# Kernel tuning notes

Hardware: AMD Instinct MI355X
Metric: run time of the kernel (lower is better)

The kernel has to match this reference:

```python
import jax, jax.numpy as jnp
import numpy as np

N_NODES = 100_000
N_EDGES = 1_200_000


def _lap_weights(src, dst, attr, n):
    # PyG get_laplacian(sym) + ChebConv scaling with lambda_max=2.0:
    # L_hat = (2/lmax)(I - D^-1/2 A D^-1/2) - I = -D^-1/2 A D^-1/2 (zero diagonal)
    deg = jnp.zeros((n,), attr.dtype).at[src].add(attr)
    dis = jnp.where(deg > 0, jax.lax.rsqrt(jnp.maximum(deg, 1e-30)), 0.0)
    return -(dis[src] * attr * dis[dst])


def _prop(x, src, dst, lw, n):
    # y_i = sum_{(j->i)} lw_e * x_j   (gather -> scale -> scatter-add)
    return jnp.zeros((n, x.shape[1]), x.dtype).at[dst].add(lw[:, None] * x[src])


def _cheb(x, src, dst, lw, W, b):
    # W: [K, F_in, F_out]; Tx0 = x, Tx1 = L_hat x (K<=2 here)
    out = x @ W[0]
    if W.shape[0] > 1:
        tx1 = _prop(x, src, dst, lw, x.shape[0])
        out = out + tx1 @ W[1]
    return out + b


def setup_inputs() -> dict:
    key = jax.random.key(0)
    ks = jax.random.split(key, 11)
    x = jax.random.normal(ks[0], (N_NODES, 20), jnp.float32)
    edge_index = jax.random.randint(ks[1], (2, N_EDGES), 0, N_NODES, jnp.int32)
    attr = jax.random.uniform(ks[2], (N_EDGES,), jnp.float32)
    def glorot(k, shape):
        fan = shape[-2] + shape[-1]
        return jax.random.normal(k, shape, jnp.float32) * jnp.sqrt(2.0 / fan)
    return {
        "x": x, "edge_index": edge_index, "attr": attr,
        "w1": glorot(ks[3], (1, 20, 32)), "b1": jnp.zeros((32,), jnp.float32),
        "w2": glorot(ks[4], (2, 32, 64)), "b2": jnp.zeros((64,), jnp.float32),
        "w3": glorot(ks[5], (2, 64, 2)), "b3": jnp.zeros((2,), jnp.float32),
        "gate_w": glorot(ks[6], (2, 1)), "gate_b": jnp.zeros((1,), jnp.float32),
    }


def reference(x, edge_index, attr, w1, b1, w2, b2, w3, b3, gate_w, gate_b):
    n = x.shape[0]
    src, dst = edge_index[0], edge_index[1]
    lw = _lap_weights(src, dst, attr, n)
    h = jax.nn.leaky_relu(_cheb(x, src, dst, lw, w1, b1))   # [N, 32]
    h = jax.nn.leaky_relu(_cheb(h, src, dst, lw, w2, b2))   # [N, 64]
    h = _cheb(h, src, dst, lw, w3, b3)                       # [N, 2]
    # GlobalAttention with batch = zeros (single graph): softmax over nodes
    gate = jax.nn.softmax(h @ gate_w + gate_b, axis=0)       # [N, 1]
    pooled = jnp.sum(gate * h, axis=0, keepdims=True)        # [1, 2]
    return jax.nn.log_softmax(pooled, axis=1)
```

## Files before the change

kernel.cpp:

```cpp
#include <hip/hip_runtime.h>
#include <hip/hip_bf16.h>
#include <math.h>

#define N_NODES 100000
#define N_EDGES 1200000
#define E4 (N_EDGES / 4)
#define G2B ((N_NODES + 255) / 256)
#define NB_L1 G2B
#define RANGE 12800
#define NRANGE 8
#define CHK 32
#define NB_DEG (NRANGE * CHK)
#define GPC ((E4 + CHK - 1) / CHK)
#define NBIN 391
#define BINCAP 3584
#define NB_P1 256
#define GP1 ((E4 + NB_P1 - 1) / NB_P1)
#define WQ (8.f * 32767.f)

__device__ __forceinline__ float disf(float d) {
    return (d > 0.f) ? rsqrtf(d) : 0.f;
}

__global__ void degbin_kernel(const int4* __restrict__ src4, const float4* __restrict__ attr4,
                              float* __restrict__ partial) {
    __shared__ float ldeg[RANGE];
    int rb = blockIdx.x;
    int r = rb / CHK;
    int c = rb - r * CHK;
    int base = r * RANGE;
    for (int j = threadIdx.x; j < RANGE; j += blockDim.x) ldeg[j] = 0.f;
    __syncthreads();
    int g0 = c * GPC;
    int g1 = g0 + GPC; if (g1 > E4) g1 = E4;
    for (int g = g0 + threadIdx.x; g < g1; g += blockDim.x) {
        int4 s = src4[g];
        float4 a = attr4[g];
        unsigned o;
        o = (unsigned)(s.x - base); if (o < RANGE) atomicAdd(&ldeg[o], a.x);
        o = (unsigned)(s.y - base); if (o < RANGE) atomicAdd(&ldeg[o], a.y);
        o = (unsigned)(s.z - base); if (o < RANGE) atomicAdd(&ldeg[o], a.z);
        o = (unsigned)(s.w - base); if (o < RANGE) atomicAdd(&ldeg[o], a.w);
    }
    __syncthreads();
    float* dstp = partial + (size_t)rb * RANGE;
    for (int j = threadIdx.x; j < RANGE; j += blockDim.x) dstp[j] = ldeg[j];
}

__global__ void degred_kernel(const float* __restrict__ partial, float* __restrict__ deg) {
    int i = blockIdx.x * blockDim.x + threadIdx.x;
    if (i >= N_NODES) return;
    int r = i / RANGE;
    int j = i - r * RANGE;
    const float* p = partial + (size_t)r * CHK * RANGE + j;
    float s = 0.f;
#pragma unroll
    for (int c = 0; c < CHK; c++) s += p[(size_t)c * RANGE];
    deg[i] = s;
}

__global__ void p1l1_kernel(const int4* __restrict__ src4, const int4* __restrict__ dst4,
                            const float4* __restrict__ attr4, const float* __restrict__ deg,
                            const float* __restrict__ x, const float* __restrict__ w1,
                            const float* __restrict__ b1,
                            int* __restrict__ binCursor, uint2* __restrict__ binRegion,
                            signed char* __restrict__ h1q, float* __restrict__ sscale) {
    __shared__ int lhist[NBIN];
    __shared__ int lbase[NBIN];
    __shared__ int lcnt[NBIN];
    __shared__ float sw[20 * 32];
    __shared__ float sb[32];

    if (blockIdx.x < NB_P1) {
        int g0 = blockIdx.x * GP1;
        int g1 = g0 + GP1; if (g1 > E4) g1 = E4;
        for (int j = threadIdx.x; j < NBIN; j += blockDim.x) { lhist[j] = 0; lcnt[j] = 0; }
        __syncthreads();
        for (int g = g0 + threadIdx.x; g < g1; g += blockDim.x) {
            int4 d = dst4[g];
            atomicAdd(&lhist[d.x >> 8], 1);
            atomicAdd(&lhist[d.y >> 8], 1);
            atomicAdd(&lhist[d.z >> 8], 1);
            atomicAdd(&lhist[d.w >> 8], 1);
        }
        __syncthreads();
        for (int j = threadIdx.x; j < NBIN; j += blockDim.x)
            lbase[j] = (lhist[j] > 0) ? atomicAdd(&binCursor[j], lhist[j]) : 0;
        __syncthreads();
        for (int g = g0 + threadIdx.x; g < g1; g += blockDim.x) {
            int4 s = src4[g];
            int4 d = dst4[g];
            float4 a = attr4[g];
            {
                int bin = d.x >> 8;
                float w = a.x * disf(deg[s.x]);
                int pos = lbase[bin] + atomicAdd(&lcnt[bin], 1);
                if (pos < BINCAP)
                    binRegion[(size_t)bin * BINCAP + pos] =
                        make_uint2(((unsigned)s.x << 8) | (unsigned)(d.x & 255), __float_as_uint(w));
            }
            {
                int bin = d.y >> 8;
                float w = a.y * disf(deg[s.y]);
                int pos = lbase[bin] + atomicAdd(&lcnt[bin], 1);
                if (pos < BINCAP)
                    binRegion[(size_t)bin * BINCAP + pos] =
                        make_uint2(((unsigned)s.y << 8) | (unsigned)(d.y & 255), __float_as_uint(w));
            }
            {
                int bin = d.z >> 8;
                float w = a.z * disf(deg[s.z]);
                int pos = lbase[bin] + atomicAdd(&lcnt[bin], 1);
                if (pos < BINCAP)
                    binRegion[(size_t)bin * BINCAP + pos] =
                        make_uint2(((unsigned)s.z << 8) | (unsigned)(d.z & 255), __float_as_uint(w));
            }
            {
                int bin = d.w >> 8;
                float w = a.w * disf(deg[s.w]);
                int pos = lbase[bin] + atomicAdd(&lcnt[bin], 1);
                if (pos < BINCAP)
                    binRegion[(size_t)bin * BINCAP + pos] =
                        make_uint2(((unsigned)s.w << 8) | (unsigned)(d.w & 255), __float_as_uint(w));
            }
        }
    } else {
        for (int t = threadIdx.x; t < 20 * 32; t += blockDim.x) sw[t] = w1[t];
        if (threadIdx.x < 32) sb[threadIdx.x] = b1[threadIdx.x];
        __syncthreads();
        int i = (blockIdx.x - NB_P1) * blockDim.x + threadIdx.x;
        if (i >= N_NODES) return;
        float xr[20];
#pragma unroll
        for (int k = 0; k < 20; k++) xr[k] = x[(size_t)i * 20 + k];
        float row[32];
        float rmax = 0.f;
#pragma unroll
        for (int j = 0; j < 32; j++) {
            float a = sb[j];
#pragma unroll
            for (int k = 0; k < 20; k++) a += xr[k] * sw[k * 32 + j];
            a = (a > 0.f) ? a : 0.01f * a;
            row[j] = a;
            rmax = fmaxf(rmax, fabsf(a));
        }
        float sc = fmaxf(rmax * (1.f / 127.f), 1e-4f);
        float inv = 1.f / sc;
        sscale[i] = sc;
#pragma unroll
        for (int j = 0; j < 32; j++) {
            h1q[(size_t)i * 32 + j] = (signed char)lrintf(row[j] * inv);
        }
    }
}

__global__ void binscan_kernel(const int* __restrict__ binCursor, int* __restrict__ bin_start) {
    __shared__ int sm[512];
    int t = threadIdx.x;
    int v = 0;
    if (t < NBIN) {
        v = binCursor[t];
        if (v > BINCAP) v = BINCAP;
    }
    sm[t] = v;
    __syncthreads();
    for (int off = 1; off < 512; off <<= 1) {
        int u = (t >= off) ? sm[t - off] : 0;
        __syncthreads();
        sm[t] += u;
        __syncthreads();
    }
    if (t < NBIN) bin_start[t + 1] = sm[t];
    if (t == 0) bin_start[0] = 0;
}

__global__ void p2_kernel(const uint2* __restrict__ binRegion, const int* __restrict__ bin_start,
                          const float* __restrict__ sscale,
                          int* __restrict__ row_start, unsigned* __restrict__ csr) {
    __shared__ uint2 recs[BINCAP];
    __shared__ int hist[256];
    __shared__ int excl[256];
    __shared__ int cnt[256];
    int b = blockIdx.x;
    int t = threadIdx.x;
    int base = bin_start[b];
    int c = bin_start[b + 1] - base;
    const uint2* reg = binRegion + (size_t)b * BINCAP;
    for (int j = t; j < c; j += 256) recs[j] = reg[j];
    hist[t] = 0; cnt[t] = 0;
    __syncthreads();
    for (int j = t; j < c; j += 256) atomicAdd(&hist[recs[j].x & 255u], 1);
    __syncthreads();
    int v = hist[t];
    excl[t] = v;
    __syncthreads();
    for (int off = 1; off < 256; off <<= 1) {
        int u = (t >= off) ? excl[t - off] : 0;
        __syncthreads();
        excl[t] += u;
        __syncthreads();
    }
    int ex = excl[t] - v;
    row_start[b * 256 + t] = base + ex;
    if (b == NBIN - 1 && t == 255) row_start[NBIN * 256] = bin_start[NBIN];
    __syncthreads();
    hist[t] = ex;
    __syncthreads();
    for (int j = t; j < c; j += 256) {
        unsigned w0 = recs[j].x;
        int low = (int)(w0 & 255u);
        int src = (int)(w0 >> 8);
        float w = __uint_as_float(recs[j].y);
        float ws = w * sscale[src] * WQ;
        unsigned q = (unsigned)(ws + 0.5f);
        if (q > 32767u) q = 32767u;
        int pos = hist[low] + atomicAdd(&cnt[low], 1);
        csr[base + pos] = ((unsigned)src << 15) | q;
    }
}

__global__ void gl2_kernel(const int* __restrict__ row_start, const unsigned* __restrict__ csr,
                           const float* __restrict__ deg, const signed char* __restrict__ h1q,
                           const float* __restrict__ sscale,
                           const float* __restrict__ w2, const float* __restrict__ b2,
                           const float* __restrict__ w3,
                           float2* __restrict__ z0, float2* __restrict__ z1w) {
    __shared__ float s0[32 * 64];
    __shared__ float s1[32 * 64];
    __shared__ float sw3[256];
    __shared__ float sb[64];
    __shared__ float h1s[8][32];
    __shared__ float t1s[8][32];
    for (int t = threadIdx.x; t < 32 * 64; t += blockDim.x) {
        s0[t] = w2[t];
        s1[t] = w2[32 * 64 + t];
    }
    for (int t = threadIdx.x; t < 256; t += blockDim.x) sw3[t] = w3[t];
    if (threadIdx.x < 64) sb[threadIdx.x] = b2[threadIdx.x];
    __syncthreads();

    int grp = threadIdx.x >> 5;
    int lane = threadIdx.x & 31;
    int e4 = lane >> 3;
    int fg = lane & 7;
    int node = blockIdx.x * 8 + grp;
    bool alive = (node < N_NODES);

    int acc0 = 0, acc1 = 0, acc2 = 0, acc3 = 0;
    if (alive) {
        int rs = row_start[node], re = row_start[node + 1];
        int j = rs + e4;
        for (; j + 4 < re; j += 8) {
            unsigned ea = csr[j];
            unsigned eb = csr[j + 4];
            int sa  = (int)(ea >> 15);
            int sbn = (int)(eb >> 15);
            int wqa = (int)(ea & 0x7FFFu);
            int wqb = (int)(eb & 0x7FFFu);
            int pa = *reinterpret_cast<const int*>(h1q + (size_t)sa  * 32 + fg * 4);
            int pb = *reinterpret_cast<const int*>(h1q + (size_t)sbn * 32 + fg * 4);
            acc0 += wqa * (int)(signed char)(pa)        + wqb * (int)(signed char)(pb);
            acc1 += wqa * (int)(signed char)(pa >> 8)   + wqb * (int)(signed char)(pb >> 8);
            acc2 += wqa * (int)(signed char)(pa >> 16)  + wqb * (int)(signed char)(pb >> 16);
            acc3 += wqa * (int)(signed char)(pa >> 24)  + wqb * (int)(signed char)(pb >> 24);
        }
        if (j < re) {
            unsigned ea = csr[j];
            int sa  = (int)(ea >> 15);
            int wqa = (int)(ea & 0x7FFFu);
            int pa = *reinterpret_cast<const int*>(h1q + (size_t)sa * 32 + fg * 4);
            acc0 += wqa * (int)(signed char)(pa);
            acc1 += wqa * (int)(signed char)(pa >> 8);
            acc2 += wqa * (int)(signed char)(pa >> 16);
            acc3 += wqa * (int)(signed char)(pa >> 24);
        }
    }
    acc0 += __shfl_xor(acc0, 8);  acc0 += __shfl_xor(acc0, 16);
    acc1 += __shfl_xor(acc1, 8);  acc1 += __shfl_xor(acc1, 16);
    acc2 += __shfl_xor(acc2, 8);  acc2 += __shfl_xor(acc2, 16);
    acc3 += __shfl_xor(acc3, 8);  acc3 += __shfl_xor(acc3, 16);

    if (alive && e4 == 0) {
        float dn = -disf(deg[node]) * (1.f / WQ);
        int packed = *reinterpret_cast<const int*>(h1q + (size_t)node * 32 + fg * 4);
        float sc = sscale[node];
        h1s[grp][fg * 4 + 0] = sc * (float)(signed char)(packed);
        h1s[grp][fg * 4 + 1] = sc * (float)(signed char)(packed >> 8);
        h1s[grp][fg * 4 + 2] = sc * (float)(signed char)(packed >> 16);
        h1s[grp][fg * 4 + 3] = sc * (float)(signed char)(packed >> 24);
        t1s[grp][fg * 4 + 0] = dn * (float)acc0;
        t1s[grp][fg * 4 + 1] = dn * (float)acc1;
        t1s[grp][fg * 4 + 2] = dn * (float)acc2;
        t1s[grp][fg * 4 + 3] = dn * (float)acc3;
    }
    __syncthreads();

    int f = lane;
    float a0 = sb[f], a1 = sb[f + 32];
#pragma unroll 8
    for (int k = 0; k < 32; k++) {
        float h = h1s[grp][k];
        float tv = t1s[grp][k];
        a0 += h * s0[k * 64 + f]      + tv * s1[k * 64 + f];
        a1 += h * s0[k * 64 + f + 32] + tv * s1[k * 64 + f + 32];
    }
    float v0 = (a0 > 0.f) ? a0 : 0.01f * a0;
    float v1 = (a1 > 0.f) ? a1 : 0.01f * a1;

    float z00 = v0 * sw3[f * 2 + 0] + v1 * sw3[(f + 32) * 2 + 0];
    float z01 = v0 * sw3[f * 2 + 1] + v1 * sw3[(f + 32) * 2 + 1];
    float z10 = v0 * sw3[128 + f * 2 + 0] + v1 * sw3[128 + (f + 32) * 2 + 0];
    float z11 = v0 * sw3[128 + f * 2 + 1] + v1 * sw3[128 + (f + 32) * 2 + 1];
#pragma unroll
    for (int m = 16; m > 0; m >>= 1) {
        z00 += __shfl_xor(z00, m);
        z01 += __shfl_xor(z01, m);
        z10 += __shfl_xor(z10, m);
        z11 += __shfl_xor(z11, m);
    }
    if (alive && f == 0) {
        z0[node] = make_float2(z00, z01);
        float isc = 1.f / sscale[node];
        z1w[node] = make_float2(z10 * isc, z11 * isc);
    }
}

__global__ void g2acc_kernel(const int* __restrict__ row_start, const unsigned* __restrict__ csr,
                             const float* __restrict__ deg,
                             const float2* __restrict__ z0, const float2* __restrict__ z1w,
                             const float* __restrict__ b3, const float* __restrict__ gw,
                             const float* __restrict__ gb, float4* __restrict__ quads) {
    __shared__ float sm[256], ss[256], s0[256], s1[256];
    int t = threadIdx.x;
    int i = blockIdx.x * blockDim.x + t;
    float m = -INFINITY, se = 0.f, a0 = 0.f, a1 = 0.f;
    if (i < N_NODES) {
        int rs = row_start[i], re = row_start[i + 1];
        float acc0 = 0.f, acc1 = 0.f;
        for (int j = rs; j < re; j++) {
            unsigned e = csr[j];
            int s = (int)(e >> 15);
            float wq = (float)(e & 0x7FFFu);
            float2 zv = z1w[s];
            acc0 += wq * zv.x;
            acc1 += wq * zv.y;
        }
        float di = -disf(deg[i]) * (1.f / WQ);
        float2 z0v = z0[i];
        float o0 = z0v.x + di * acc0 + b3[0];
        float o1 = z0v.y + di * acc1 + b3[1];
        m = o0 * gw[0] + o1 * gw[1] + gb[0];
        se = 1.f; a0 = o0; a1 = o1;
    }
    sm[t] = m; ss[t] = se; s0[t] = a0; s1[t] = a1;
    __syncthreads();
    for (int s = 128; s > 0; s >>= 1) {
        if (t < s) {
            float mb = sm[t + s];
            if (mb != -INFINITY) {
                float ma = sm[t];
                if (ma == -INFINITY) {
                    sm[t] = mb; ss[t] = ss[t + s]; s0[t] = s0[t + s]; s1[t] = s1[t + s];
                } else if (mb <= ma) {
                    float c = __expf(mb - ma);
                    ss[t] += ss[t + s] * c;
                    s0[t] += s0[t + s] * c;
                    s1[t] += s1[t + s] * c;
                } else {
                    float c = __expf(ma - mb);
                    ss[t] = ss[t] * c + ss[t + s];
                    s0[t] = s0[t] * c + s0[t + s];
                    s1[t] = s1[t] * c + s1[t + s];
                    sm[t] = mb;
                }
            }
        }
        __syncthreads();
    }
    if (t == 0) quads[blockIdx.x] = make_float4(sm[0], ss[0], s0[0], s1[0]);
}

__global__ void accB_kernel(const float4* __restrict__ quads, float* __restrict__ out) {
    __shared__ float sm[512], ss[512], s0[512], s1[512];
    int t = threadIdx.x;
    float m = -INFINITY, se = 0.f, a0 = 0.f, a1 = 0.f;
    if (t < G2B) {
        float4 q = quads[t];
        m = q.x; se = q.y; a0 = q.z; a1 = q.w;
    }
    sm[t] = m; ss[t] = se; s0[t] = a0; s1[t] = a1;
    __syncthreads();
    for (int s = 256; s > 0; s >>= 1) {
        if (t < s) {
            float mb = sm[t + s];
            if (mb != -INFINITY) {
                float ma = sm[t];
                if (ma == -INFINITY) {
                    sm[t] = mb; ss[t] = ss[t + s]; s0[t] = s0[t + s]; s1[t] = s1[t + s];
                } else if (mb <= ma) {
                    float c = __expf(mb - ma);
                    ss[t] += ss[t + s] * c;
                    s0[t] += s0[t + s] * c;
                    s1[t] += s1[t + s] * c;
                } else {
                    float c = __expf(ma - mb);
                    ss[t] = ss[t] * c + ss[t + s];
                    s0[t] = s0[t] * c + s0[t + s];
                    s1[t] = s1[t] * c + s1[t + s];
                    sm[t] = mb;
                }
            }
        }
        __syncthreads();
    }
    if (t == 0) {
        float se0 = ss[0];
        float p0 = s0[0] / se0;
        float p1 = s1[0] / se0;
        float mm = fmaxf(p0, p1);
        float l = mm + logf(__expf(p0 - mm) + __expf(p1 - mm));
        out[0] = p0 - l;
        out[1] = p1 - l;
    }
}

extern "C" void kernel_launch(void* const* d_in, const int* in_sizes, int n_in,
                              void* d_out, int out_size, void* d_ws, size_t ws_size,
                              hipStream_t stream) {
    const float* x    = (const float*)d_in[0];
    const int*   ei   = (const int*)d_in[1];
    const float* attr = (const float*)d_in[2];
    const float* w1   = (const float*)d_in[3];
    const float* b1   = (const float*)d_in[4];
    const float* w2   = (const float*)d_in[5];
    const float* b2   = (const float*)d_in[6];
    const float* w3   = (const float*)d_in[7];
    const float* b3   = (const float*)d_in[8];
    const float* gw   = (const float*)d_in[9];
    const float* gb   = (const float*)d_in[10];
    float* out = (float*)d_out;

    const int4*   src4  = (const int4*)ei;
    const int4*   dst4  = (const int4*)(ei + N_EDGES);
    const float4* attr4 = (const float4*)attr;

    float* ws = (float*)d_ws;
    size_t off = 0;
    int*      binCursor = (int*)(ws + off); off += NBIN;
    int*      bin_start = (int*)(ws + off); off += NBIN + 1;
    float*    deg       = ws + off; off += N_NODES;
    float*    sscale    = ws + off; off += N_NODES;
    int*      row_start = (int*)(ws + off); off += NBIN * 256 + 1;
    float*    partial   = ws + off; off += (size_t)NB_DEG * RANGE;
    off = (off + 3) & ~(size_t)3;
    uint2*    binRegion = (uint2*)(ws + off); off += (size_t)NBIN * BINCAP * 2;
    unsigned* csr       = (unsigned*)(ws + off); off += N_EDGES;
    signed char* h1q    = (signed char*)(ws + off); off += (size_t)N_NODES * 8;
    float2*   z0  = (float2*)(ws + off); off += (size_t)N_NODES * 2;
    float2*   z1w = (float2*)(ws + off); off += (size_t)N_NODES * 2;
    off = (off + 3) & ~(size_t)3;
    float4*   quads = (float4*)(ws + off); off += (size_t)G2B * 4;

    const int B = 256;
    auto cdiv = [](long long a, long long b) { return (int)((a + b - 1) / b); };

    hipMemsetAsync(binCursor, 0, NBIN * sizeof(int), stream);

    degbin_kernel<<<NB_DEG, B, 0, stream>>>(src4, attr4, partial);
    degred_kernel<<<cdiv(N_NODES, B), B, 0, stream>>>(partial, deg);

    p1l1_kernel<<<NB_P1 + NB_L1, B, 0, stream>>>(src4, dst4, attr4, deg, x, w1, b1,
                                                 binCursor, binRegion, h1q, sscale);

    binscan_kernel<<<1, 512, 0, stream>>>(binCursor, bin_start);

    p2_kernel<<<NBIN, B, 0, stream>>>(binRegion, bin_start, sscale, row_start, csr);

    gl2_kernel<<<cdiv(N_NODES, 8), B, 0, stream>>>(row_start, csr, deg, h1q, sscale,
                                                   w2, b2, w3, z0, z1w);

    g2acc_kernel<<<G2B, B, 0, stream>>>(row_start, csr, deg, z0, z1w, b3, gw, gb, quads);

    accB_kernel<<<1, 512, 0, stream>>>(quads, out);
}
```

Before: 160.7 us.

## Split layer-2 gather from dense transform into separate gather and batched GEMM kernels

Splits the fused layer-2 kernel in two. The first kernel only gathers quantized neighbour features into int32 sums and writes them to a new buffer. The second loads 64 nodes per block with swizzled transposed weights and register-blocks 4 nodes per thread to reuse weight reads. Previously each block of 8 nodes reloaded all W2 into shared memory and did a per-node matvec. The cost is a 12.8MB intermediate round-trip through global memory plus an extra kernel launch.

```diff
diff --git a/kernel.cpp b/kernel.cpp
--- a/kernel.cpp
+++ b/kernel.cpp
@@ -17,6 +17,8 @@
 #define NB_P1 256
 #define GP1 ((E4 + NB_P1 - 1) / NB_P1)
 #define WQ (8.f * 32767.f)
+#define DNS_NPB 64
+#define NB_DNS ((N_NODES + DNS_NPB - 1) / DNS_NPB)
 
 __device__ __forceinline__ float disf(float d) {
     return (d > 0.f) ? rsqrtf(d) : 0.f;
@@ -219,109 +221,145 @@
     }
 }
 
-__global__ void gl2_kernel(const int* __restrict__ row_start, const unsigned* __restrict__ csr,
-                           const float* __restrict__ deg, const signed char* __restrict__ h1q,
-                           const float* __restrict__ sscale,
-                           const float* __restrict__ w2, const float* __restrict__ b2,
-                           const float* __restrict__ w3,
-                           float2* __restrict__ z0, float2* __restrict__ z1w) {
-    __shared__ float s0[32 * 64];
-    __shared__ float s1[32 * 64];
-    __shared__ float sw3[256];
-    __shared__ float sb[64];
-    __shared__ float h1s[8][32];
-    __shared__ float t1s[8][32];
-    for (int t = threadIdx.x; t < 32 * 64; t += blockDim.x) {
-        s0[t] = w2[t];
-        s1[t] = w2[32 * 64 + t];
-    }
-    for (int t = threadIdx.x; t < 256; t += blockDim.x) sw3[t] = w3[t];
-    if (threadIdx.x < 64) sb[threadIdx.x] = b2[threadIdx.x];
-    __syncthreads();
-
+__global__ void gth_kernel(const int* __restrict__ row_start, const unsigned* __restrict__ csr,
+                           const signed char* __restrict__ h1q, int* __restrict__ t1i) {
     int grp = threadIdx.x >> 5;
     int lane = threadIdx.x & 31;
     int e4 = lane >> 3;
     int fg = lane & 7;
     int node = blockIdx.x * 8 + grp;
-    bool alive = (node < N_NODES);
+    if (node >= N_NODES) return;
 
     int acc0 = 0, acc1 = 0, acc2 = 0, acc3 = 0;
-    if (alive) {
-        int rs = row_start[node], re = row_start[node + 1];
-        int j = rs + e4;
-        for (; j + 4 < re; j += 8) {
-            unsigned ea = csr[j];
-            unsigned eb = csr[j + 4];
-            int sa  = (int)(ea >> 15);
-            int sbn = (int)(eb >> 15);
-            int wqa = (int)(ea & 0x7FFFu);
-            int wqb = (int)(eb & 0x7FFFu);
-            int pa = *reinterpret_cast<const int*>(h1q + (size_t)sa  * 32 + fg * 4);
-            int pb = *reinterpret_cast<const int*>(h1q + (size_t)sbn * 32 + fg * 4);
-            acc0 += wqa * (int)(signed char)(pa)        + wqb * (int)(signed char)(pb);
-            acc1 += wqa * (int)(signed char)(pa >> 8)   + wqb * (int)(signed char)(pb >> 8);
-            acc2 += wqa * (int)(signed char)(pa >> 16)  + wqb * (int)(signed char)(pb >> 16);
-            acc3 += wqa * (int)(signed char)(pa >> 24)  + wqb * (int)(signed char)(pb >> 24);
-        }
-        if (j < re) {
-            unsigned ea = csr[j];
-            int sa  = (int)(ea >> 15);
-            int wqa = (int)(ea & 0x7FFFu);
-            int pa = *reinterpret_cast<const int*>(h1q + (size_t)sa * 32 + fg * 4);
-            acc0 += wqa * (int)(signed char)(pa);
-            acc1 += wqa * (int)(signed char)(pa >> 8);
-            acc2 += wqa * (int)(signed char)(pa >> 16);
-            acc3 += wqa * (int)(signed char)(pa >> 24);
-        }
+    int rs = row_start[node], re = row_start[node + 1];
+    int j = rs + e4;
+    for (; j + 4 < re; j += 8) {
+        unsigned ea = csr[j];
+        unsigned eb = csr[j + 4];
+        int sa  = (int)(ea >> 15);
+        int sbn = (int)(eb >> 15);
+        int wqa = (int)(ea & 0x7FFFu);
+        int wqb = (int)(eb & 0x7FFFu);
+        int pa = *reinterpret_cast<const int*>(h1q + (size_t)sa  * 32 + fg * 4);
+        int pb = *reinterpret_cast<const int*>(h1q + (size_t)sbn * 32 + fg * 4);
+        acc0 += wqa * (int)(signed char)(pa)        + wqb * (int)(signed char)(pb);
+        acc1 += wqa * (int)(signed char)(pa >> 8)   + wqb * (int)(signed char)(pb >> 8);
+        acc2 += wqa * (int)(signed char)(pa >> 16)  + wqb * (int)(signed char)(pb >> 16);
+        acc3 += wqa * (int)(signed char)(pa >> 24)  + wqb * (int)(signed char)(pb >> 24);
+    }
+    if (j < re) {
+        unsigned ea = csr[j];
+        int sa  = (int)(ea >> 15);
+        int wqa = (int)(ea & 0x7FFFu);
+        int pa = *reinterpret_cast<const int*>(h1q + (size_t)sa * 32 + fg * 4);
+        acc0 += wqa * (int)(signed char)(pa);
+        acc1 += wqa * (int)(signed char)(pa >> 8);
+        acc2 += wqa * (int)(signed char)(pa >> 16);
+        acc3 += wqa * (int)(signed char)(pa >> 24);
     }
     acc0 += __shfl_xor(acc0, 8);  acc0 += __shfl_xor(acc0, 16);
     acc1 += __shfl_xor(acc1, 8);  acc1 += __shfl_xor(acc1, 16);
     acc2 += __shfl_xor(acc2, 8);  acc2 += __shfl_xor(acc2, 16);
     acc3 += __shfl_xor(acc3, 8);  acc3 += __shfl_xor(acc3, 16);
-
-    if (alive && e4 == 0) {
-        float dn = -disf(deg[node]) * (1.f / WQ);
-        int packed = *reinterpret_cast<const int*>(h1q + (size_t)node * 32 + fg * 4);
-        float sc = sscale[node];
-        h1s[grp][fg * 4 + 0] = sc * (float)(signed char)(packed);
-        h1s[grp][fg * 4 + 1] = sc * (float)(signed char)(packed >> 8);
-        h1s[grp][fg * 4 + 2] = sc * (float)(signed char)(packed >> 16);
-        h1s[grp][fg * 4 + 3] = sc * (float)(signed char)(packed >> 24);
-        t1s[grp][fg * 4 + 0] = dn * (float)acc0;
-        t1s[grp][fg * 4 + 1] = dn * (float)acc1;
-        t1s[grp][fg * 4 + 2] = dn * (float)acc2;
-        t1s[grp][fg * 4 + 3] = dn * (float)acc3;
-    }
-    __syncthreads();
-
-    int f = lane;
-    float a0 = sb[f], a1 = sb[f + 32];
-#pragma unroll 8
-    for (int k = 0; k < 32; k++) {
-        float h = h1s[grp][k];
-        float tv = t1s[grp][k];
-        a0 += h * s0[k * 64 + f]      + tv * s1[k * 64 + f];
-        a1 += h * s0[k * 64 + f + 32] + tv * s1[k * 64 + f + 32];
-    }
-    float v0 = (a0 > 0.f) ? a0 : 0.01f * a0;
-    float v1 = (a1 > 0.f) ? a1 : 0.01f * a1;
-
-    float z00 = v0 * sw3[f * 2 + 0] + v1 * sw3[(f + 32) * 2 + 0];
-    float z01 = v0 * sw3[f * 2 + 1] + v1 * sw3[(f + 32) * 2 + 1];
-    float z10 = v0 * sw3[128 + f * 2 + 0] + v1 * sw3[128 + (f + 32) * 2 + 0];
-    float z11 = v0 * sw3[128 + f * 2 + 1] + v1 * sw3[128 + (f + 32) * 2 + 1];
+    if (e4 == 0) {
+        reinterpret_cast<int4*>(t1i)[(size_t)node * 8 + fg] = make_int4(acc0, acc1, acc2, acc3);
+    }
+}
+
+__global__ void dns_kernel(const int* __restrict__ t1i, const signed char* __restrict__ h1q,
+                           const float* __restrict__ sscale, const float* __restrict__ deg,
+                           const float* __restrict__ w2, const float* __restrict__ b2,
+                           const float* __restrict__ w3,
+                           float2* __restrict__ z0, float2* __restrict__ z1w) {
+    __shared__ float s0T[64][32];
+    __shared__ float s1T[64][32];
+    __shared__ float sw3[256];
+    __shared__ float sb[64];
+    __shared__ float hf[DNS_NPB][32];
+    __shared__ float tf[DNS_NPB][32];
+    __shared__ float iscs[DNS_NPB];
+    int tid = threadIdx.x;
+    int base = blockIdx.x * DNS_NPB;
+
+    for (int t = tid; t < 2048; t += 256) {
+        int f = t >> 5;
+        int jj = t & 31;
+        int k = jj ^ ((f & 7) << 2);
+        s0T[f][jj] = w2[k * 64 + f];
+        s1T[f][jj] = w2[2048 + k * 64 + f];
+    }
+    for (int t = tid; t < 256; t += 256) sw3[t] = w3[t];
+    if (tid < 64) sb[tid] = b2[tid];
+    for (int idx = tid; idx < DNS_NPB * 32; idx += 256) {
+        int n = idx >> 5, k = idx & 31;
+        int node = base + n;
+        if (node < N_NODES) {
+            hf[n][k] = sscale[node] * (float)h1q[(size_t)node * 32 + k];
+            tf[n][k] = -disf(deg[node]) * (1.f / WQ) * (float)t1i[(size_t)node * 32 + k];
+        } else {
+            hf[n][k] = 0.f;
+            tf[n][k] = 0.f;
+        }
+    }
+    if (tid < DNS_NPB) {
+        int node = base + tid;
+        iscs[tid] = (node < N_NODES) ? 1.f / sscale[node] : 1.f;
+    }
+    __syncthreads();
+
+    int f = tid & 63;
+    int quad = tid >> 6;
+    for (int round = 0; round < 4; ++round) {
+        int q4 = (round * 4 + quad) * 4;
+        float a0 = sb[f], a1 = sb[f], a2 = sb[f], a3 = sb[f];
 #pragma unroll
-    for (int m = 16; m > 0; m >>= 1) {
-        z00 += __shfl_xor(z00, m);
-        z01 += __shfl_xor(z01, m);
-        z10 += __shfl_xor(z10, m);
-        z11 += __shfl_xor(z11, m);
-    }
-    if (alive && f == 0) {
-        z0[node] = make_float2(z00, z01);
-        float isc = 1.f / sscale[node];
-        z1w[node] = make_float2(z10 * isc, z11 * isc);
+        for (int k = 0; k < 32; k += 4) {
+            int ks = k ^ ((f & 7) << 2);
+            float4 w0 = *reinterpret_cast<const float4*>(&s0T[f][ks]);
+            float4 w1 = *reinterpret_cast<const float4*>(&s1T[f][ks]);
+            float4 h0 = *reinterpret_cast<const float4*>(&hf[q4 + 0][k]);
+            float4 t0 = *reinterpret_cast<const float4*>(&tf[q4 + 0][k]);
+            float4 h1 = *reinterpret_cast<const float4*>(&hf[q4 + 1][k]);
+            float4 t1 = *reinterpret_cast<const float4*>(&tf[q4 + 1][k]);
+            float4 h2 = *reinterpret_cast<const float4*>(&hf[q4 + 2][k]);
+            float4 t2 = *reinterpret_cast<const float4*>(&tf[q4 + 2][k]);
+            float4 h3 = *reinterpret_cast<const float4*>(&hf[q4 + 3][k]);
+            float4 t3 = *reinterpret_cast<const float4*>(&tf[q4 + 3][k]);
+            a0 += h0.x * w0.x + h0.y * w0.y + h0.z * w0.z + h0.w * w0.w
+                + t0.x * w1.x + t0.y * w1.y + t0.z * w1.z + t0.w * w1.w;
+            a1 += h1.x * w0.x + h1.y * w0.y + h1.z * w0.z + h1.w * w0.w
+                + t1.x * w1.x + t1.y * w1.y + t1.z * w1.z + t1.w * w1.w;
+            a2 += h2.x * w0.x + h2.y * w0.y + h2.z * w0.z + h2.w * w0.w
+                + t2.x * w1.x + t2.y * w1.y + t2.z * w1.z + t2.w * w1.w;
+            a3 += h3.x * w0.x + h3.y * w0.y + h3.z * w0.z + h3.w * w0.w
+                + t3.x * w1.x + t3.y * w1.y + t3.z * w1.z + t3.w * w1.w;
+        }
+#define EPILOG(aV, qq) {                                                        \
+            float v = (aV > 0.f) ? aV : 0.01f * aV;                             \
+            float z00 = v * sw3[f * 2 + 0];                                     \
+            float z01 = v * sw3[f * 2 + 1];                                     \
+            float z10 = v * sw3[128 + f * 2 + 0];                               \
+            float z11 = v * sw3[128 + f * 2 + 1];                               \
+            for (int m = 32; m > 0; m >>= 1) {                                  \
+                z00 += __shfl_xor(z00, m);                                      \
+                z01 += __shfl_xor(z01, m);                                      \
+                z10 += __shfl_xor(z10, m);                                      \
+                z11 += __shfl_xor(z11, m);                                      \
+            }                                                                   \
+            if (f == 0) {                                                       \
+                int node = base + q4 + qq;                                      \
+                if (node < N_NODES) {                                           \
+                    z0[node] = make_float2(z00, z01);                           \
+                    float isc = iscs[q4 + qq];                                  \
+                    z1w[node] = make_float2(z10 * isc, z11 * isc);              \
+                }                                                               \
+            }                                                                   \
+        }
+        EPILOG(a0, 0)
+        EPILOG(a1, 1)
+        EPILOG(a2, 2)
+        EPILOG(a3, 3)
+#undef EPILOG
     }
 }
 
@@ -456,6 +494,8 @@
     uint2*    binRegion = (uint2*)(ws + off); off += (size_t)NBIN * BINCAP * 2;
     unsigned* csr       = (unsigned*)(ws + off); off += N_EDGES;
     signed char* h1q    = (signed char*)(ws + off); off += (size_t)N_NODES * 8;
+    off = (off + 3) & ~(size_t)3;
+    int*      t1i       = (int*)(ws + off); off += (size_t)N_NODES * 32;
     float2*   z0  = (float2*)(ws + off); off += (size_t)N_NODES * 2;
     float2*   z1w = (float2*)(ws + off); off += (size_t)N_NODES * 2;
     off = (off + 3) & ~(size_t)3;
@@ -476,8 +516,9 @@
 
     p2_kernel<<<NBIN, B, 0, stream>>>(binRegion, bin_start, sscale, row_start, csr);
 
-    gl2_kernel<<<cdiv(N_NODES, 8), B, 0, stream>>>(row_start, csr, deg, h1q, sscale,
-                                                   w2, b2, w3, z0, z1w);
+    gth_kernel<<<cdiv(N_NODES, 8), B, 0, stream>>>(row_start, csr, h1q, t1i);
+
+    dns_kernel<<<NB_DNS, B, 0, stream>>>(t1i, h1q, sscale, deg, w2, b2, w3, z0, z1w);
 
     g2acc_kernel<<<G2B, B, 0, stream>>>(row_start, csr, deg, z0, z1w, b3, gw, gb, quads);
 
```

After: 547.1 us. 240% more time.
